# Performance work log

Measured on AMD Instinct MI355X. Metric: run time of the kernel, lower is better.

The kernel has to match this reference:

```python
import jax, jax.numpy as jnp
import numpy as np

SOS_TOKEN = 1


def gru_cell(x, h, Wih, Whh, bih, bhh):
    # torch.nn.GRU gate math; x:[B,H], h:[B,H]; Wih/Whh:[3H,H]
    gi = x @ Wih.T + bih
    gh = h @ Whh.T + bhh
    ir, iz, inn = jnp.split(gi, 3, axis=-1)
    hr, hz, hn = jnp.split(gh, 3, axis=-1)
    r = jax.nn.sigmoid(ir + hr)
    z = jax.nn.sigmoid(iz + hz)
    n = jnp.tanh(inn + r * hn)
    return (1.0 - z) * n + z * h


def setup_inputs() -> dict:
    key = jax.random.key(0)
    ks = jax.random.split(key, 20)
    B, S, T, V, H = 32, 512, 128, 32000, 512
    sc = 0.08
    p = lambda i, shape: (jax.random.normal(ks[i], shape, jnp.float32) * sc)
    return {
        "input_seq": jax.random.randint(ks[0], (B, S), 0, V),
        "target_seq": jax.random.randint(ks[1], (B, T), 0, V),
        "emb": p(2, (V, H)),
        "ef_Wih": p(3, (3 * H, H)), "ef_Whh": p(4, (3 * H, H)),
        "ef_bih": p(5, (3 * H,)), "ef_bhh": p(6, (3 * H,)),
        "eb_Wih": p(7, (3 * H, H)), "eb_Whh": p(8, (3 * H, H)),
        "eb_bih": p(9, (3 * H,)), "eb_bhh": p(10, (3 * H,)),
        "d_Wih": p(11, (3 * H, H)), "d_Whh": p(12, (3 * H, H)),
        "d_bih": p(13, (3 * H,)), "d_bhh": p(14, (3 * H,)),
        "att_W": p(15, (H, 2 * H)), "att_b": p(16, (H,)),
        "out_W": p(17, (V, H)), "out_b": p(18, (V,)),
    }


def reference(input_seq, target_seq, emb,
              ef_Wih, ef_Whh, ef_bih, ef_bhh,
              eb_Wih, eb_Whh, eb_bih, eb_bhh,
              d_Wih, d_Whh, d_bih, d_bhh,
              att_W, att_b, out_W, out_b):
    B, S = input_seq.shape
    T = target_seq.shape[1]
    H = emb.shape[1]
    dtype = emb.dtype

    # ---- encoder: bidirectional GRU over source ----
    xs = jnp.swapaxes(emb[input_seq], 0, 1)  # [S,B,H]
    h0 = jnp.zeros((B, H), dtype)

    def make_step(Wih, Whh, bih, bhh):
        def f(h, xt):
            hn = gru_cell(xt, h, Wih, Whh, bih, bhh)
            return hn, hn
        return f

    hf_last, out_f = jax.lax.scan(make_step(ef_Wih, ef_Whh, ef_bih, ef_bhh), h0, xs)
    hb_last, out_bwd = jax.lax.scan(make_step(eb_Wih, eb_Whh, eb_bih, eb_bhh), h0, xs[::-1])
    out_bwd = out_bwd[::-1]
    # encoder_output[:, :H] + encoder_output[:, H:]  == sum of directions
    enc_out = jnp.swapaxes(out_f + out_bwd, 0, 1)  # [B,S,H]
    # decoder_hidden = encoder_hidden[-1,0] + encoder_hidden[-1,1]
    h_dec0 = hf_last + hb_last  # [B,H]

    # ---- greedy decode for T steps with argmax feedback ----
    tgt = target_seq.T  # [T,B]
    tok0 = jnp.full((B,), SOS_TOKEN, target_seq.dtype)
    batch_idx = jnp.arange(B)

    def dec_step(carry, tgt_t):
        h, tok, loss = carry
        xt = emb[tok]                                   # [B,H]
        hn = gru_cell(xt, h, d_Wih, d_Whh, d_bih, d_bhh)
        scores = jnp.einsum('bh,bsh->bs', hn, enc_out)  # dot attention
        w = jax.nn.softmax(scores, axis=-1)
        ctx = jnp.einsum('bs,bsh->bh', w, enc_out)
        att_out = jnp.tanh(jnp.concatenate([ctx, hn], axis=-1) @ att_W.T + att_b)
        logits = att_out @ out_W.T + out_b              # [B,V]
        logp = jax.nn.log_softmax(logits, axis=-1)
        loss = loss - logp[batch_idx, tgt_t]            # -log softmax(output)[target]
        nxt = jnp.argmax(logits, axis=-1).astype(tok.dtype)
        return (hn, nxt, loss), None

    init = (h_dec0, tok0, jnp.zeros((B,), dtype))
    (_, _, loss), _ = jax.lax.scan(dec_step, init, tgt)
    # mean over examples of (per-example loss / decoding_cnt)
    return jnp.mean(loss / T)
```

## Files before the change

### kernel.cpp

```cpp
#include <hip/hip_runtime.h>
#include <math.h>

#define B 32
#define S 512
#define T 128
#define V 32000
#define H 512
#define NB 256
#define NTE 512
#define NTD 256
#define LCHUNK 250
#define LROWS 128

__device__ __forceinline__ float dot4(float acc, float4 a, float4 b){
    return fmaf(a.x,b.x, fmaf(a.y,b.y, fmaf(a.z,b.z, fmaf(a.w,b.w, acc))));
}
__device__ __forceinline__ float sigmoidf_(float x){ return 1.0f/(1.0f+expf(-x)); }

template<int GRPSZ>
__device__ __forceinline__ void gbar_arrive(unsigned* bb, unsigned grp, unsigned n){
    __syncthreads();
    if (threadIdx.x == 0){
        const unsigned r = __hip_atomic_fetch_add(bb + grp*32, 1u,
                              __ATOMIC_RELEASE, __HIP_MEMORY_SCOPE_AGENT);
        if (r == n*(unsigned)GRPSZ - 1u){
            const unsigned q = __hip_atomic_fetch_add(bb + 256, 1u,
                                  __ATOMIC_RELEASE, __HIP_MEMORY_SCOPE_AGENT);
            if (q == n*8u - 1u)
                __hip_atomic_store(bb + 288, n,
                                   __ATOMIC_RELEASE, __HIP_MEMORY_SCOPE_AGENT);
        }
    }
}
__device__ __forceinline__ void gbar_wait(unsigned* bb, unsigned n){
    if (threadIdx.x == 0){
        long guard = 0;
        while (__hip_atomic_load(bb + 288, __ATOMIC_RELAXED, __HIP_MEMORY_SCOPE_AGENT) < n){
            __builtin_amdgcn_s_sleep(2);
            if (++guard > 200000000L) break;
        }
        (void)__hip_atomic_load(bb + 288, __ATOMIC_ACQUIRE, __HIP_MEMORY_SCOPE_AGENT);
    }
    __syncthreads();
}

__global__ __launch_bounds__(NTE, 1) void enc_persistent(
    const int* __restrict__ input_seq, const float* __restrict__ emb,
    const float* __restrict__ fWih, const float* __restrict__ fWhh,
    const float* __restrict__ fbih, const float* __restrict__ fbhh,
    const float* __restrict__ bWih, const float* __restrict__ bWhh,
    const float* __restrict__ bbih, const float* __restrict__ bbhh,
    float* enc_out, float* out_b, unsigned* bars)
{
    __shared__ float wlds[24*512];
    __shared__ float shp[3*128*6];
    const int bk = blockIdx.x, tid = threadIdx.x;
    const int dir = bk & 1, jg = bk >> 1;
    const int b = tid & 31, jj = (tid>>5)&3, kh = tid>>7;
    const int j = jg*4 + jj;
    const unsigned grp = ((unsigned)jg) & 7u;

    const float *Wih = dir? bWih : fWih;
    const float *Whh = dir? bWhh : fWhh;
    const float *bih = dir? bbih : fbih;
    const float *bhh = dir? bbhh : fbhh;
    float* outp = dir? out_b : enc_out;
    unsigned* bar = bars + dir*1024;

    for (int r=0;r<24;r++){
        const int jr = jg*4 + (r/6);
        const int g  = r % 6;
        const float* src = (g<3) ? (Wih + ((size_t)g*H + jr)*H)
                                 : (Whh + ((size_t)(g-3)*H + jr)*H);
        for (int k=tid;k<H;k+=NTE) wlds[r*512+k] = src[k];
    }
    __syncthreads();

    const float4* wx0 = (const float4*)(wlds + (jj*6+0)*512 + kh*128);
    const float4* wx1 = (const float4*)(wlds + (jj*6+1)*512 + kh*128);
    const float4* wx2 = (const float4*)(wlds + (jj*6+2)*512 + kh*128);
    const float4* wh0 = (const float4*)(wlds + (jj*6+3)*512 + kh*128);
    const float4* wh1 = (const float4*)(wlds + (jj*6+4)*512 + kh*128);
    const float4* wh2 = (const float4*)(wlds + (jj*6+5)*512 + kh*128);
    const float bi_r = bih[j], bi_z = bih[H+j], bi_n = bih[2*H+j];
    const float bh_r = bhh[j], bh_z = bhh[H+j], bh_n = bhh[2*H+j];

    for (int t=0; t<S; t++){
        const int pos  = dir ? (S-1-t) : t;
        const int hpos = dir ? (S-t)   : (t-1);
        const int tokb = input_seq[b*S + pos];
        const float4* x4 = (const float4*)(emb + (size_t)tokb*H + kh*128);

        float ir=0.f, iz=0.f, in_=0.f;
        #pragma unroll 8
        for (int k=0;k<32;k++){
            const float4 xv = x4[k];
            ir  = dot4(ir , xv, wx0[k]);
            iz  = dot4(iz , xv, wx1[k]);
            in_ = dot4(in_, xv, wx2[k]);
        }

        if (t > 0) gbar_wait(bar, (unsigned)t);

        float hr=0.f, hz=0.f, hn=0.f;
        if (t > 0){
            const float4* h4 = (const float4*)(outp + ((size_t)b*S + hpos)*H + kh*128);
            #pragma unroll 8
            for (int k=0;k<32;k++){
                const float4 hv = h4[k];
                hr = dot4(hr, hv, wh0[k]);
                hz = dot4(hz, hv, wh1[k]);
                hn = dot4(hn, hv, wh2[k]);
            }
        }
        if (kh){
            float* p = shp + ((kh-1)*128 + jj*32 + b)*6;
            p[0]=ir; p[1]=iz; p[2]=in_; p[3]=hr; p[4]=hz; p[5]=hn;
        }
        __syncthreads();
        if (!kh){
            #pragma unroll
            for (int q=0;q<3;q++){
                const float* p = shp + (q*128 + jj*32 + b)*6;
                ir+=p[0]; iz+=p[1]; in_+=p[2]; hr+=p[3]; hz+=p[4]; hn+=p[5];
            }
            float hprev = (t>0) ? outp[((size_t)b*S + hpos)*H + j] : 0.0f;
            const float r = sigmoidf_(ir + bi_r + hr + bh_r);
            const float z = sigmoidf_(iz + bi_z + hz + bh_z);
            const float n = tanhf(in_ + bi_n + r*(hn + bh_n));
            outp[((size_t)b*S + pos)*H + j] = (1.0f - z)*n + z*hprev;
        }
        gbar_arrive<16>(bar, grp, (unsigned)(t+1));
    }
}

__global__ __launch_bounds__(NTD, 1) void dec_persistent(
    const int* __restrict__ target_seq, const float* __restrict__ emb,
    const float* __restrict__ dWih, const float* __restrict__ dWhh,
    const float* __restrict__ dbih, const float* __restrict__ dbhh,
    const float* __restrict__ attW, const float* __restrict__ attb,
    const float* __restrict__ outW, const float* __restrict__ outBias,
    float* enc_out, const float* out_b,
    float* hdec, float* scores, float* ctxb, float* att_out,
    float* pm, float* ps, int* pidx, float* lossb,
    float* out, unsigned* bar)
{
    __shared__ __align__(16) float smem[128*32*4];
    __shared__ float wg[12*512];
    __shared__ float wp[2*1024];
    __shared__ float red_m[4][32], red_s[4][32];
    __shared__ int   red_i[4][32];
    __shared__ int sh_tok[B];
    const int bk = blockIdx.x, tid = threadIdx.x;
    const unsigned grp = (unsigned)bk & 7u;
    unsigned bn = 1;
#define GSYNC() do { gbar_arrive<32>(bar, grp, bn); gbar_wait(bar, bn); ++bn; } while(0)

    for (int r=0;r<12;r++){
        const int jr = bk*2 + (r/6);
        const int g  = r % 6;
        const float* src = (g<3) ? (dWih + ((size_t)g*H + jr)*H)
                                 : (dWhh + ((size_t)(g-3)*H + jr)*H);
        for (int k=tid;k<H;k+=NTD) wg[r*512+k] = src[k];
    }
    for (int r=0;r<2;r++){
        const float* src = attW + (size_t)(bk*2+r)*(2*H);
        for (int k=tid;k<2*H;k+=NTD) wp[r*1024+k] = src[k];
    }

    {
        const int gid = bk*NTD + tid;
        if (gid < B*H){
            const int bb = gid >> 9, jq = gid & 511;
            hdec[gid] = enc_out[((size_t)bb*S + (S-1))*H + jq] + out_b[((size_t)bb*S)*H + jq];
        }
        if (bk==0 && tid<B) lossb[tid] = 0.0f;
    }
    GSYNC();

    {
        float4* e4 = (float4*)enc_out; const float4* o4 = (const float4*)out_b;
        for (size_t i = (size_t)bk*NTD + tid; i < (size_t)B*S*H/4; i += (size_t)NB*NTD){
            float4 x = e4[i]; const float4 y = o4[i];
            x.x+=y.x; x.y+=y.y; x.z+=y.z; x.w+=y.w; e4[i]=x;
        }
    }
    GSYNC();

    const int gb = tid & 31, gj = (tid>>5)&1, gkq = tid>>6;
    const int jrow = bk*2 + gj;
    const float4* gwir = (const float4*)(wg + (gj*6+0)*512 + gkq*128);
    const float4* gwiz = (const float4*)(wg + (gj*6+1)*512 + gkq*128);
    const float4* gwin = (const float4*)(wg + (gj*6+2)*512 + gkq*128);
    const float4* gwhr = (const float4*)(wg + (gj*6+3)*512 + gkq*128);
    const float4* gwhz = (const float4*)(wg + (gj*6+4)*512 + gkq*128);
    const float4* gwhn = (const float4*)(wg + (gj*6+5)*512 + gkq*128);
    const float gbi_r = dbih[jrow], gbi_z = dbih[H+jrow], gbi_n = dbih[2*H+jrow];
    const float gbh_r = dbhh[jrow], gbh_z = dbhh[H+jrow], gbh_n = dbhh[2*H+jrow];
    const float4* pw = (const float4*)(wp + gj*1024 + gkq*256);

    for (int t=0; t<T; t++){
        float* hin  = hdec + (size_t)(t&1)*B*H;
        float* hout = hdec + (size_t)((t+1)&1)*B*H;

        if (t == 0){
            if (tid < B) sh_tok[tid] = 1;
        } else {
            const int mb = tid>>3, p = tid&7;
            float bv = -INFINITY; int ai = 0x7FFFFFFF;
            for (int c=p; c<LCHUNK; c+=8){
                const float v = pm[mb*LCHUNK + c];
                if (v > bv){ bv = v; ai = pidx[mb*LCHUNK + c]; }
            }
            #pragma unroll
            for (int m=1; m<8; m<<=1){
                const float ov = __shfl_xor(bv, m); const int oi = __shfl_xor(ai, m);
                if (ov > bv || (ov == bv && oi < ai)){ bv = ov; ai = oi; }
            }
            if (p==0) sh_tok[mb] = ai;
            if (bk == 0){
                float mm = -INFINITY;
                for (int c=p; c<LCHUNK; c+=8) mm = fmaxf(mm, pm[mb*LCHUNK+c]);
                #pragma unroll
                for (int m=1;m<8;m<<=1) mm = fmaxf(mm, __shfl_xor(mm, m));
                float se = 0.0f;
                for (int c=p; c<LCHUNK; c+=8) se += ps[mb*LCHUNK+c]*expf(pm[mb*LCHUNK+c]-mm);
                #pragma unroll
                for (int m=1;m<8;m<<=1) se += __shfl_xor(se, m);
                const int tg = target_seq[mb*T + (t-1)];
                const float4* ar = (const float4*)(att_out + (size_t)mb*H) + p*16;
                const float4* wr = (const float4*)(outW + (size_t)tg*H) + p*16;
                float d = 0.0f;
                #pragma unroll
                for (int k=0;k<16;k++) d = dot4(d, ar[k], wr[k]);
                #pragma unroll
                for (int m=1;m<8;m<<=1) d += __shfl_xor(d, m);
                if (p==0) lossb[mb] += (mm + logf(se)) - (d + outBias[tg]);
            }
        }
        __syncthreads();
        {
            const int tokb = sh_tok[gb];
            const float4* x4 = (const float4*)(emb + (size_t)tokb*H + gkq*128);
            const float4* h4 = (const float4*)(hin + (size_t)gb*H + gkq*128);
            float ir=0.f, iz=0.f, in_=0.f, hr=0.f, hz=0.f, hn=0.f;
            #pragma unroll 4
            for (int k=0;k<32;k++){
                const float4 xv = x4[k], hv = h4[k];
                ir  = dot4(ir , xv, gwir[k]);
                iz  = dot4(iz , xv, gwiz[k]);
                in_ = dot4(in_, xv, gwin[k]);
                hr  = dot4(hr , hv, gwhr[k]);
                hz  = dot4(hz , hv, gwhz[k]);
                hn  = dot4(hn , hv, gwhn[k]);
            }
            if (gkq){
                float* pp = smem + ((gkq-1)*64 + gj*32 + gb)*6;
                pp[0]=ir; pp[1]=iz; pp[2]=in_; pp[3]=hr; pp[4]=hz; pp[5]=hn;
            }
            __syncthreads();
            if (!gkq){
                #pragma unroll
                for (int q=0;q<3;q++){
                    const float* pp = smem + (q*64 + gj*32 + gb)*6;
                    ir+=pp[0]; iz+=pp[1]; in_+=pp[2]; hr+=pp[3]; hz+=pp[4]; hn+=pp[5];
                }
                const float r = sigmoidf_(ir + gbi_r + hr + gbh_r);
                const float z = sigmoidf_(iz + gbi_z + hz + gbh_z);
                const float n = tanhf(in_ + gbi_n + r*(hn + gbh_n));
                const float hprev = hin[(size_t)gb*H + jrow];
                hout[(size_t)gb*H + jrow] = (1.0f - z)*n + z*hprev;
            }
        }
        GSYNC();

        {
            const int bS = bk & 31, sg = bk >> 5;
            const int sl = tid>>2, q = tid&3;
            const int s = sg*64 + sl;
            const float4* h4 = (const float4*)(hout + (size_t)bS*H + q*128);
            const float4* e4 = (const float4*)(enc_out + ((size_t)bS*S + s)*H + q*128);
            float a = 0.f;
            #pragma unroll 8
            for (int k=0;k<32;k++) a = dot4(a, h4[k], e4[k]);
            a += __shfl_xor(a, 1);
            a += __shfl_xor(a, 2);
            if (q == 0) scores[bS*S + s] = a;
        }
        GSYNC();

        {
            const int bC = bk & 31, cg = bk >> 5;
            float* sh_w = smem; float* red = smem + 512; float* part = smem + 768;
            const float s0 = scores[bC*S + tid], s1 = scores[bC*S + tid + 256];
            red[tid] = fmaxf(s0,s1); __syncthreads();
            for (int off=128; off>0; off>>=1){ if (tid<off) red[tid]=fmaxf(red[tid],red[tid+off]); __syncthreads(); }
            const float M = red[0]; __syncthreads();
            const float e0 = expf(s0-M), e1 = expf(s1-M);
            red[tid] = e0+e1; __syncthreads();
            for (int off=128; off>0; off>>=1){ if (tid<off) red[tid]+=red[tid+off]; __syncthreads(); }
            const float inv = 1.0f/red[0];
            __syncthreads();
            sh_w[tid] = e0*inv; sh_w[tid+256] = e1*inv;
            __syncthreads();
            const int col = cg*64 + (tid & 63);
            const int sg2 = tid >> 6;
            const float* Ec = enc_out + (size_t)bC*S*H + col;
            float acc = 0.f;
            #pragma unroll 8
            for (int s2=sg2; s2<S; s2+=4) acc = fmaf(sh_w[s2], Ec[(size_t)s2*H], acc);
            part[tid] = acc; __syncthreads();
            if (tid < 64) ctxb[bC*512 + col] = part[tid]+part[tid+64]+part[tid+128]+part[tid+192];
        }
        GSYNC();

        {
            const float* act = (gkq < 2) ? (ctxb + (size_t)gb*512 + gkq*256)
                                         : (hout + (size_t)gb*H + (gkq-2)*256);
            const float4* a4 = (const float4*)act;
            float acc = 0.f;
            #pragma unroll 8
            for (int k=0;k<64;k++) acc = dot4(acc, a4[k], pw[k]);
            if (gkq){
                smem[(gkq-1)*64 + gj*32 + gb] = acc;
            }
            __syncthreads();
            if (!gkq){
                acc += smem[0*64 + gj*32 + gb] + smem[1*64 + gj*32 + gb] + smem[2*64 + gj*32 + gb];
                att_out[(size_t)gb*H + jrow] = tanhf(acc + attb[jrow]);
            }
        }
        GSYNC();

        if (bk < LCHUNK){
            float4* sh4 = (float4*)smem;
            for (int idx = tid; idx < 32*128; idx += NTD){
                const int k4 = idx & 127, bb = idx >> 7;
                sh4[k4*32 + bb] = ((const float4*)att_out)[(size_t)bb*128 + k4];
            }
            __syncthreads();
            const int wid = tid >> 6, lane = tid & 63;
            const int rl = lane & 7, bl = lane >> 3;
            const int r0 = bk*LROWS + wid*32 + rl*4;
            const float4* w0 = (const float4*)(outW + (size_t)(r0+0)*H);
            const float4* w1 = (const float4*)(outW + (size_t)(r0+1)*H);
            const float4* w2 = (const float4*)(outW + (size_t)(r0+2)*H);
            const float4* w3 = (const float4*)(outW + (size_t)(r0+3)*H);
            float acc[4][4];
            #pragma unroll
            for (int i=0;i<4;i++){ acc[i][0]=0.f; acc[i][1]=0.f; acc[i][2]=0.f; acc[i][3]=0.f; }
            #pragma unroll 4
            for (int k=0;k<128;k++){
                const float4 a0 = sh4[k*32 + bl*4 + 0];
                const float4 a1 = sh4[k*32 + bl*4 + 1];
                const float4 a2 = sh4[k*32 + bl*4 + 2];
                const float4 a3 = sh4[k*32 + bl*4 + 3];
                {   const float4 wv = w0[k];
                    acc[0][0]=dot4(acc[0][0],wv,a0); acc[0][1]=dot4(acc[0][1],wv,a1);
                    acc[0][2]=dot4(acc[0][2],wv,a2); acc[0][3]=dot4(acc[0][3],wv,a3); }
                {   const float4 wv = w1[k];
                    acc[1][0]=dot4(acc[1][0],wv,a0); acc[1][1]=dot4(acc[1][1],wv,a1);
                    acc[1][2]=dot4(acc[1][2],wv,a2); acc[1][3]=dot4(acc[1][3],wv,a3); }
                {   const float4 wv = w2[k];
                    acc[2][0]=dot4(acc[2][0],wv,a0); acc[2][1]=dot4(acc[2][1],wv,a1);
                    acc[2][2]=dot4(acc[2][2],wv,a2); acc[2][3]=dot4(acc[2][3],wv,a3); }
                {   const float4 wv = w3[k];
                    acc[3][0]=dot4(acc[3][0],wv,a0); acc[3][1]=dot4(acc[3][1],wv,a1);
                    acc[3][2]=dot4(acc[3][2],wv,a2); acc[3][3]=dot4(acc[3][3],wv,a3); }
            }
            const float bs0 = outBias[r0], bs1 = outBias[r0+1], bs2 = outBias[r0+2], bs3 = outBias[r0+3];
            #pragma unroll
            for (int j=0;j<4;j++){
                const float l0 = acc[0][j]+bs0, l1 = acc[1][j]+bs1, l2 = acc[2][j]+bs2, l3 = acc[3][j]+bs3;
                float M = l0; int bi = r0;
                if (l1 > M){ M=l1; bi=r0+1; }
                if (l2 > M){ M=l2; bi=r0+2; }
                if (l3 > M){ M=l3; bi=r0+3; }
                float Ssum = expf(l0-M)+expf(l1-M)+expf(l2-M)+expf(l3-M);
                #pragma unroll
                for (int m=1;m<8;m<<=1){
                    const float oM = __shfl_xor(M, m);
                    const float oS = __shfl_xor(Ssum, m);
                    const int   oI = __shfl_xor(bi, m);
                    const float nM = fmaxf(M, oM);
                    const float nS = Ssum*expf(M-nM) + oS*expf(oM-nM);
                    if (oM > M || (oM == M && oI < bi)) bi = oI;
                    M = nM; Ssum = nS;
                }
                if (rl == 0){
                    red_m[wid][bl*4+j] = M;
                    red_s[wid][bl*4+j] = Ssum;
                    red_i[wid][bl*4+j] = bi;
                }
            }
            __syncthreads();
            if (tid < 32){
                float M = red_m[0][tid], Ssum = red_s[0][tid]; int bi = red_i[0][tid];
                #pragma unroll
                for (int w=1; w<4; w++){
                    const float oM = red_m[w][tid], oS = red_s[w][tid]; const int oI = red_i[w][tid];
                    const float nM = fmaxf(M, oM);
                    const float nS = Ssum*expf(M-nM) + oS*expf(oM-nM);
                    if (oM > M || (oM == M && oI < bi)) bi = oI;
                    M = nM; Ssum = nS;
                }
                pm[tid*LCHUNK + bk] = M;
                ps[tid*LCHUNK + bk] = Ssum;
                pidx[tid*LCHUNK + bk] = bi;
            }
        }
        GSYNC();
    }

    if (bk == 0){
        const int mb = tid>>3, p = tid&7;
        float mm = -INFINITY;
        for (int c=p; c<LCHUNK; c+=8) mm = fmaxf(mm, pm[mb*LCHUNK+c]);
        #pragma unroll
        for (int m=1;m<8;m<<=1) mm = fmaxf(mm, __shfl_xor(mm, m));
        float se = 0.0f;
        for (int c=p; c<LCHUNK; c+=8) se += ps[mb*LCHUNK+c]*expf(pm[mb*LCHUNK+c]-mm);
        #pragma unroll
        for (int m=1;m<8;m<<=1) se += __shfl_xor(se, m);
        const int tg = target_seq[mb*T + (T-1)];
        const float4* ar = (const float4*)(att_out + (size_t)mb*H) + p*16;
        const float4* wr = (const float4*)(outW + (size_t)tg*H) + p*16;
        float d = 0.0f;
        #pragma unroll
        for (int k=0;k<16;k++) d = dot4(d, ar[k], wr[k]);
        #pragma unroll
        for (int m=1;m<8;m<<=1) d += __shfl_xor(d, m);
        if (p==0) lossb[mb] += (mm + logf(se)) - (d + outBias[tg]);
        __syncthreads();
        if (tid < B){
            float v = lossb[tid];
            for (int off=16; off>0; off>>=1) v += __shfl_down(v, off);
            if (tid == 0) out[0] = v / (float)(B*T);
        }
    }
#undef GSYNC
}

extern "C" void kernel_launch(void* const* d_in, const int* in_sizes, int n_in,
                              void* d_out, int out_size, void* d_ws, size_t ws_size,
                              hipStream_t stream)
{
    const int*   input_seq  = (const int*)  d_in[0];
    const int*   target_seq = (const int*)  d_in[1];
    const float* emb    = (const float*)d_in[2];
    const float* efWih  = (const float*)d_in[3];
    const float* efWhh  = (const float*)d_in[4];
    const float* efbih  = (const float*)d_in[5];
    const float* efbhh  = (const float*)d_in[6];
    const float* ebWih  = (const float*)d_in[7];
    const float* ebWhh  = (const float*)d_in[8];
    const float* ebbih  = (const float*)d_in[9];
    const float* ebbhh  = (const float*)d_in[10];
    const float* dWih   = (const float*)d_in[11];
    const float* dWhh   = (const float*)d_in[12];
    const float* dbih   = (const float*)d_in[13];
    const float* dbhh   = (const float*)d_in[14];
    const float* attW   = (const float*)d_in[15];
    const float* attb   = (const float*)d_in[16];
    const float* outW   = (const float*)d_in[17];
    const float* outBias= (const float*)d_in[18];

    float* ws      = (float*)d_ws;
    unsigned* bars = (unsigned*)ws;
    float* enc_out = ws + 4096;
    float* outb    = enc_out + (size_t)B*S*H;
    float* scores  = outb    + (size_t)B*S*H;
    float* ctxb    = scores  + (size_t)B*S;
    float* attout  = ctxb    + (size_t)B*512;
    float* pm      = attout  + (size_t)B*H;
    float* ps      = pm      + (size_t)B*LCHUNK;
    int*   pidx    = (int*)(ps + (size_t)B*LCHUNK);
    float* hdec    = (float*)(pidx + (size_t)B*LCHUNK);
    float* lossb   = hdec    + (size_t)2*B*H;

    hipMemsetAsync(bars, 0, 16384, stream);

    enc_persistent<<<NB, NTE, 0, stream>>>(input_seq, emb,
        efWih, efWhh, efbih, efbhh, ebWih, ebWhh, ebbih, ebbhh,
        enc_out, outb, bars);

    dec_persistent<<<NB, NTD, 0, stream>>>(target_seq, emb,
        dWih, dWhh, dbih, dbhh, attW, attb, outW, outBias,
        enc_out, outb, hdec, scores, ctxb, attout,
        pm, ps, pidx, lossb, (float*)d_out, bars + 2048);
}
```

Measured before the change: 31.84 ms.

## Restructure decoder so one block per batch row does GRU, attention, projection locally

```diff
diff --git a/kernel.cpp b/kernel.cpp
--- a/kernel.cpp
+++ b/kernel.cpp
@@ -8,9 +8,10 @@
 #define H 512
 #define NB 256
 #define NTE 512
-#define NTD 256
+#define NTD 1024
 #define LCHUNK 250
 #define LROWS 128
+#define BPITCH 49
 
 __device__ __forceinline__ float dot4(float acc, float4 a, float4 b){
     return fmaf(a.x,b.x, fmaf(a.y,b.y, fmaf(a.z,b.z, fmaf(a.w,b.w, acc))));
@@ -141,40 +142,35 @@
     const float* __restrict__ attW, const float* __restrict__ attb,
     const float* __restrict__ outW, const float* __restrict__ outBias,
     float* enc_out, const float* out_b,
-    float* hdec, float* scores, float* ctxb, float* att_out,
-    float* pm, float* ps, int* pidx, float* lossb,
+    float* att_out, float* pm, float* ps, int* pidx, float* lossb,
     float* out, unsigned* bar)
 {
-    __shared__ __align__(16) float smem[128*32*4];
-    __shared__ float wg[12*512];
-    __shared__ float wp[2*1024];
-    __shared__ float red_m[4][32], red_s[4][32];
-    __shared__ int   red_i[4][32];
-    __shared__ int sh_tok[B];
+    __shared__ __align__(16) float smem[128*BPITCH*4];
+    __shared__ __align__(16) float P_H[2*512];
+    __shared__ __align__(16) float P_AO[512];
+    __shared__ float P_LOSS;
+    __shared__ int   P_TOK;
+    __shared__ float BR_M[8][32], BR_S[8][32];
+    __shared__ int   BR_I[8][32];
+
+    float* A_X   = smem;
+    float* A_P6  = smem + 512;
+    float* A_SC  = smem + 3584;
+    float* A_P1  = smem + 4096;
+    float* A_CTX = smem + 4608;
+    float* A_RED = smem + 5120;
+    int*   A_REDI= (int*)(smem + 5152);
+
     const int bk = blockIdx.x, tid = threadIdx.x;
     const unsigned grp = (unsigned)bk & 7u;
     unsigned bn = 1;
 #define GSYNC() do { gbar_arrive<32>(bar, grp, bn); gbar_wait(bar, bn); ++bn; } while(0)
 
-    for (int r=0;r<12;r++){
-        const int jr = bk*2 + (r/6);
-        const int g  = r % 6;
-        const float* src = (g<3) ? (dWih + ((size_t)g*H + jr)*H)
-                                 : (dWhh + ((size_t)(g-3)*H + jr)*H);
-        for (int k=tid;k<H;k+=NTD) wg[r*512+k] = src[k];
-    }
-    for (int r=0;r<2;r++){
-        const float* src = attW + (size_t)(bk*2+r)*(2*H);
-        for (int k=tid;k<2*H;k+=NTD) wp[r*1024+k] = src[k];
-    }
-
-    {
-        const int gid = bk*NTD + tid;
-        if (gid < B*H){
-            const int bb = gid >> 9, jq = gid & 511;
-            hdec[gid] = enc_out[((size_t)bb*S + (S-1))*H + jq] + out_b[((size_t)bb*S)*H + jq];
-        }
-        if (bk==0 && tid<B) lossb[tid] = 0.0f;
+    if (bk < B){
+        if (tid < 512)
+            P_H[tid] = enc_out[((size_t)bk*S + (S-1))*H + tid]
+                     + out_b [((size_t)bk*S + 0    )*H + tid];
+        if (tid == 0) P_LOSS = 0.0f;
     }
     GSYNC();
 
@@ -187,147 +183,180 @@
     }
     GSYNC();
 
-    const int gb = tid & 31, gj = (tid>>5)&1, gkq = tid>>6;
-    const int jrow = bk*2 + gj;
-    const float4* gwir = (const float4*)(wg + (gj*6+0)*512 + gkq*128);
-    const float4* gwiz = (const float4*)(wg + (gj*6+1)*512 + gkq*128);
-    const float4* gwin = (const float4*)(wg + (gj*6+2)*512 + gkq*128);
-    const float4* gwhr = (const float4*)(wg + (gj*6+3)*512 + gkq*128);
-    const float4* gwhz = (const float4*)(wg + (gj*6+4)*512 + gkq*128);
-    const float4* gwhn = (const float4*)(wg + (gj*6+5)*512 + gkq*128);
-    const float gbi_r = dbih[jrow], gbi_z = dbih[H+jrow], gbi_n = dbih[2*H+jrow];
-    const float gbh_r = dbhh[jrow], gbh_z = dbhh[H+jrow], gbh_n = dbhh[2*H+jrow];
-    const float4* pw = (const float4*)(wp + gj*1024 + gkq*256);
-
     for (int t=0; t<T; t++){
-        float* hin  = hdec + (size_t)(t&1)*B*H;
-        float* hout = hdec + (size_t)((t+1)&1)*B*H;
-
-        if (t == 0){
-            if (tid < B) sh_tok[tid] = 1;
-        } else {
-            const int mb = tid>>3, p = tid&7;
-            float bv = -INFINITY; int ai = 0x7FFFFFFF;
-            for (int c=p; c<LCHUNK; c+=8){
-                const float v = pm[mb*LCHUNK + c];
-                if (v > bv){ bv = v; ai = pidx[mb*LCHUNK + c]; }
-            }
-            #pragma unroll
-            for (int m=1; m<8; m<<=1){
-                const float ov = __shfl_xor(bv, m); const int oi = __shfl_xor(ai, m);
-                if (ov > bv || (ov == bv && oi < ai)){ bv = ov; ai = oi; }
-            }
-            if (p==0) sh_tok[mb] = ai;
-            if (bk == 0){
-                float mm = -INFINITY;
-                for (int c=p; c<LCHUNK; c+=8) mm = fmaxf(mm, pm[mb*LCHUNK+c]);
+        if (bk < B){
+            const int b = bk;
+            float* ph = P_H + (t&1)*512;
+            float* pn = P_H + ((t+1)&1)*512;
+
+            if (t > 0){
+                const int tg = target_seq[b*T + (t-1)];
+                if (tid < 128){
+                    const float4 av = ((const float4*)P_AO)[tid];
+                    const float4 wv = ((const float4*)(outW + (size_t)tg*H))[tid];
+                    float d = av.x*wv.x + av.y*wv.y + av.z*wv.z + av.w*wv.w;
+                    #pragma unroll
+                    for (int m=1;m<64;m<<=1) d += __shfl_xor(d, m);
+                    if ((tid&63)==0) A_RED[16 + (tid>>6)] = d;
+                }
+                float mm = -INFINITY, zz = 0.0f, bv = -INFINITY; int ai = 0x7FFFFFFF;
+                if (tid < 256){
+                    if (tid < LCHUNK){
+                        mm = pm[b*LCHUNK + tid]; zz = ps[b*LCHUNK + tid];
+                        bv = mm; ai = pidx[b*LCHUNK + tid];
+                    }
+                    #pragma unroll
+                    for (int m=1;m<64;m<<=1){
+                        const float omm = __shfl_xor(mm, m), ozz = __shfl_xor(zz, m);
+                        const float obv = __shfl_xor(bv, m); const int oai = __shfl_xor(ai, m);
+                        if (obv > bv || (obv == bv && oai < ai)){ bv = obv; ai = oai; }
+                        const float nm = fmaxf(mm, omm);
+                        const float w1 = (mm  > -INFINITY)? expf(mm -nm) : 0.0f;
+                        const float w2 = (omm > -INFINITY)? expf(omm-nm) : 0.0f;
+                        zz = zz*w1 + ozz*w2; mm = nm;
+                    }
+                    if ((tid&63)==0){
+                        const int w = tid>>6;
+                        A_RED[w] = mm; A_RED[4+w] = zz; A_RED[8+w] = bv; A_REDI[w] = ai;
+                    }
+                }
+                __syncthreads();
+                if (tid == 0){
+                    float M = A_RED[0], Z = A_RED[4], BV = A_RED[8]; int AI = A_REDI[0];
+                    #pragma unroll
+                    for (int w=1; w<4; w++){
+                        const float oM = A_RED[w], oZ = A_RED[4+w], oB = A_RED[8+w];
+                        const int oI = A_REDI[w];
+                        if (oB > BV || (oB == BV && oI < AI)){ BV = oB; AI = oI; }
+                        const float nm = fmaxf(M, oM);
+                        const float w1 = (M  > -INFINITY)? expf(M -nm) : 0.0f;
+                        const float w2 = (oM > -INFINITY)? expf(oM-nm) : 0.0f;
+                        Z = Z*w1 + oZ*w2; M = nm;
+                    }
+                    const float d = A_RED[16] + A_RED[17];
+                    P_LOSS += (M + logf(Z)) - (d + outBias[tg]);
+                    P_TOK = AI;
+                }
+            } else {
+                if (tid == 0) P_TOK = 1;
+            }
+            __syncthreads();
+
+            {
+                const int tok = P_TOK;
+                if (tid < 128)
+                    ((float4*)A_X)[tid] = ((const float4*)(emb + (size_t)tok*H))[tid];
+            }
+            __syncthreads();
+
+            {
+                const int j = tid & 511, hf = tid >> 9;
+                const float4* x4 = (const float4*)A_X + hf*64;
+                const float4* h4 = (const float4*)ph  + hf*64;
+                const float4* wi0 = (const float4*)(dWih + ((size_t)(0*H + j))*H) + hf*64;
+                const float4* wi1 = (const float4*)(dWih + ((size_t)(1*H + j))*H) + hf*64;
+                const float4* wi2 = (const float4*)(dWih + ((size_t)(2*H + j))*H) + hf*64;
+                const float4* wh0 = (const float4*)(dWhh + ((size_t)(0*H + j))*H) + hf*64;
+                const float4* wh1 = (const float4*)(dWhh + ((size_t)(1*H + j))*H) + hf*64;
+                const float4* wh2 = (const float4*)(dWhh + ((size_t)(2*H + j))*H) + hf*64;
+                float ir=0.f, iz=0.f, in_=0.f, hr=0.f, hz=0.f, hn=0.f;
+                #pragma unroll 4
+                for (int k=0;k<64;k++){
+                    const float4 xv = x4[k], hv = h4[k];
+                    ir  = dot4(ir , xv, wi0[k]);
+                    iz  = dot4(iz , xv, wi1[k]);
+                    in_ = dot4(in_, xv, wi2[k]);
+                    hr  = dot4(hr , hv, wh0[k]);
+                    hz  = dot4(hz , hv, wh1[k]);
+                    hn  = dot4(hn , hv, wh2[k]);
+                }
+                if (hf){
+                    float* pp = A_P6 + j*6;
+                    pp[0]=ir; pp[1]=iz; pp[2]=in_; pp[3]=hr; pp[4]=hz; pp[5]=hn;
+                }
+                __syncthreads();
+                if (!hf){
+                    const float* pp = A_P6 + j*6;
+                    ir+=pp[0]; iz+=pp[1]; in_+=pp[2]; hr+=pp[3]; hz+=pp[4]; hn+=pp[5];
+                    const float r = sigmoidf_(ir + dbih[j]     + hr + dbhh[j]);
+                    const float z = sigmoidf_(iz + dbih[H+j]   + hz + dbhh[H+j]);
+                    const float n = tanhf   (in_ + dbih[2*H+j] + r*(hn + dbhh[2*H+j]));
+                    pn[j] = (1.0f - z)*n + z*ph[j];
+                }
+                __syncthreads();
+            }
+
+            {
+                const int s = tid & 511, hf = tid >> 9;
+                const float4* e4 = (const float4*)(enc_out + ((size_t)b*S + s)*H) + hf*64;
+                const float4* h4 = (const float4*)pn + hf*64;
+                float a = 0.f;
+                #pragma unroll 8
+                for (int k=0;k<64;k++) a = dot4(a, h4[k], e4[k]);
+                if (hf) A_P1[s] = a;
+                __syncthreads();
+                if (!hf) A_SC[s] = a + A_P1[s];
+                __syncthreads();
+            }
+
+            {
+                float v = (tid < 512)? A_SC[tid] : -INFINITY;
+                float vm = v;
                 #pragma unroll
-                for (int m=1;m<8;m<<=1) mm = fmaxf(mm, __shfl_xor(mm, m));
-                float se = 0.0f;
-                for (int c=p; c<LCHUNK; c+=8) se += ps[mb*LCHUNK+c]*expf(pm[mb*LCHUNK+c]-mm);
+                for (int m=1;m<64;m<<=1) vm = fmaxf(vm, __shfl_xor(vm, m));
+                if (tid < 512 && (tid&63)==0) A_RED[tid>>6] = vm;
+                __syncthreads();
+                if (tid == 0){
+                    float M = A_RED[0];
+                    #pragma unroll
+                    for (int w=1;w<8;w++) M = fmaxf(M, A_RED[w]);
+                    A_RED[8] = M;
+                }
+                __syncthreads();
+                const float M = A_RED[8];
+                const float e = (tid < 512)? expf(v - M) : 0.0f;
+                float es = e;
                 #pragma unroll
-                for (int m=1;m<8;m<<=1) se += __shfl_xor(se, m);
-                const int tg = target_seq[mb*T + (t-1)];
-                const float4* ar = (const float4*)(att_out + (size_t)mb*H) + p*16;
-                const float4* wr = (const float4*)(outW + (size_t)tg*H) + p*16;
-                float d = 0.0f;
-                #pragma unroll
-                for (int k=0;k<16;k++) d = dot4(d, ar[k], wr[k]);
-                #pragma unroll
-                for (int m=1;m<8;m<<=1) d += __shfl_xor(d, m);
-                if (p==0) lossb[mb] += (mm + logf(se)) - (d + outBias[tg]);
-            }
-        }
-        __syncthreads();
-        {
-            const int tokb = sh_tok[gb];
-            const float4* x4 = (const float4*)(emb + (size_t)tokb*H + gkq*128);
-            const float4* h4 = (const float4*)(hin + (size_t)gb*H + gkq*128);
-            float ir=0.f, iz=0.f, in_=0.f, hr=0.f, hz=0.f, hn=0.f;
-            #pragma unroll 4
-            for (int k=0;k<32;k++){
-                const float4 xv = x4[k], hv = h4[k];
-                ir  = dot4(ir , xv, gwir[k]);
-                iz  = dot4(iz , xv, gwiz[k]);
-                in_ = dot4(in_, xv, gwin[k]);
-                hr  = dot4(hr , hv, gwhr[k]);
-                hz  = dot4(hz , hv, gwhz[k]);
-                hn  = dot4(hn , hv, gwhn[k]);
-            }
-            if (gkq){
-                float* pp = smem + ((gkq-1)*64 + gj*32 + gb)*6;
-                pp[0]=ir; pp[1]=iz; pp[2]=in_; pp[3]=hr; pp[4]=hz; pp[5]=hn;
-            }
-            __syncthreads();
-            if (!gkq){
-                #pragma unroll
-                for (int q=0;q<3;q++){
-                    const float* pp = smem + (q*64 + gj*32 + gb)*6;
-                    ir+=pp[0]; iz+=pp[1]; in_+=pp[2]; hr+=pp[3]; hz+=pp[4]; hn+=pp[5];
-                }
-                const float r = sigmoidf_(ir + gbi_r + hr + gbh_r);
-                const float z = sigmoidf_(iz + gbi_z + hz + gbh_z);
-                const float n = tanhf(in_ + gbi_n + r*(hn + gbh_n));
-                const float hprev = hin[(size_t)gb*H + jrow];
-                hout[(size_t)gb*H + jrow] = (1.0f - z)*n + z*hprev;
-            }
-        }
-        GSYNC();
-
-        {
-            const int bS = bk & 31, sg = bk >> 5;
-            const int sl = tid>>2, q = tid&3;
-            const int s = sg*64 + sl;
-            const float4* h4 = (const float4*)(hout + (size_t)bS*H + q*128);
-            const float4* e4 = (const float4*)(enc_out + ((size_t)bS*S + s)*H + q*128);
-            float a = 0.f;
-            #pragma unroll 8
-            for (int k=0;k<32;k++) a = dot4(a, h4[k], e4[k]);
-            a += __shfl_xor(a, 1);
-            a += __shfl_xor(a, 2);
-            if (q == 0) scores[bS*S + s] = a;
-        }
-        GSYNC();
-
-        {
-            const int bC = bk & 31, cg = bk >> 5;
-            float* sh_w = smem; float* red = smem + 512; float* part = smem + 768;
-            const float s0 = scores[bC*S + tid], s1 = scores[bC*S + tid + 256];
-            red[tid] = fmaxf(s0,s1); __syncthreads();
-            for (int off=128; off>0; off>>=1){ if (tid<off) red[tid]=fmaxf(red[tid],red[tid+off]); __syncthreads(); }
-            const float M = red[0]; __syncthreads();
-            const float e0 = expf(s0-M), e1 = expf(s1-M);
-            red[tid] = e0+e1; __syncthreads();
-            for (int off=128; off>0; off>>=1){ if (tid<off) red[tid]+=red[tid+off]; __syncthreads(); }
-            const float inv = 1.0f/red[0];
-            __syncthreads();
-            sh_w[tid] = e0*inv; sh_w[tid+256] = e1*inv;
-            __syncthreads();
-            const int col = cg*64 + (tid & 63);
-            const int sg2 = tid >> 6;
-            const float* Ec = enc_out + (size_t)bC*S*H + col;
-            float acc = 0.f;
-            #pragma unroll 8
-            for (int s2=sg2; s2<S; s2+=4) acc = fmaf(sh_w[s2], Ec[(size_t)s2*H], acc);
-            part[tid] = acc; __syncthreads();
-            if (tid < 64) ctxb[bC*512 + col] = part[tid]+part[tid+64]+part[tid+128]+part[tid+192];
-        }
-        GSYNC();
-
-        {
-            const float* act = (gkq < 2) ? (ctxb + (size_t)gb*512 + gkq*256)
-                                         : (hout + (size_t)gb*H + (gkq-2)*256);
-            const float4* a4 = (const float4*)act;
-            float acc = 0.f;
-            #pragma unroll 8
-            for (int k=0;k<64;k++) acc = dot4(acc, a4[k], pw[k]);
-            if (gkq){
-                smem[(gkq-1)*64 + gj*32 + gb] = acc;
-            }
-            __syncthreads();
-            if (!gkq){
-                acc += smem[0*64 + gj*32 + gb] + smem[1*64 + gj*32 + gb] + smem[2*64 + gj*32 + gb];
-                att_out[(size_t)gb*H + jrow] = tanhf(acc + attb[jrow]);
+                for (int m=1;m<64;m<<=1) es += __shfl_xor(es, m);
+                if (tid < 512 && (tid&63)==0) A_RED[16 + (tid>>6)] = es;
+                __syncthreads();
+                if (tid == 0){
+                    float Z = A_RED[16];
+                    #pragma unroll
+                    for (int w=1;w<8;w++) Z += A_RED[16+w];
+                    A_RED[9] = 1.0f/Z;
+                }
+                __syncthreads();
+                if (tid < 512) A_SC[tid] = e * A_RED[9];
+                __syncthreads();
+            }
+
+            {
+                const int c = tid & 511, hf = tid >> 9;
+                const float* Ec = enc_out + (size_t)b*S*H + c;
+                float acc = 0.f;
+                const int s0 = hf*256;
+                #pragma unroll 8
+                for (int s2=s0; s2<s0+256; ++s2) acc = fmaf(A_SC[s2], Ec[(size_t)s2*H], acc);
+                if (hf) A_P1[c] = acc;
+                __syncthreads();
+                if (!hf) A_CTX[c] = acc + A_P1[c];
+                __syncthreads();
+            }
+
+            {
+                const int r = tid & 511, hf = tid >> 9;
+                const float4* aw  = (const float4*)(attW + (size_t)r*(2*H) + hf*512);
+                const float4* cat = (const float4*)(hf ? pn : A_CTX);
+                float acc = 0.f;
+                #pragma unroll 8
+                for (int k=0;k<128;k++) acc = dot4(acc, cat[k], aw[k]);
+                if (hf) A_P1[r] = acc;
+                __syncthreads();
+                if (!hf) P_AO[r] = tanhf(acc + A_P1[r] + attb[r]);
+                __syncthreads();
+                if (tid < 128)
+                    ((float4*)att_out)[(size_t)b*128 + tid] = ((const float4*)P_AO)[tid];
             }
         }
         GSYNC();
@@ -336,107 +365,123 @@
             float4* sh4 = (float4*)smem;
             for (int idx = tid; idx < 32*128; idx += NTD){
                 const int k4 = idx & 127, bb = idx >> 7;
-                sh4[k4*32 + bb] = ((const float4*)att_out)[(size_t)bb*128 + k4];
+                sh4[k4*BPITCH + (bb>>1)*3 + (bb&1)] =
+                    ((const float4*)att_out)[(size_t)bb*128 + k4];
             }
             __syncthreads();
-            const int wid = tid >> 6, lane = tid & 63;
-            const int rl = lane & 7, bl = lane >> 3;
-            const int r0 = bk*LROWS + wid*32 + rl*4;
-            const float4* w0 = (const float4*)(outW + (size_t)(r0+0)*H);
-            const float4* w1 = (const float4*)(outW + (size_t)(r0+1)*H);
-            const float4* w2 = (const float4*)(outW + (size_t)(r0+2)*H);
-            const float4* w3 = (const float4*)(outW + (size_t)(r0+3)*H);
-            float acc[4][4];
-            #pragma unroll
-            for (int i=0;i<4;i++){ acc[i][0]=0.f; acc[i][1]=0.f; acc[i][2]=0.f; acc[i][3]=0.f; }
-            #pragma unroll 4
-            for (int k=0;k<128;k++){
-                const float4 a0 = sh4[k*32 + bl*4 + 0];
-                const float4 a1 = sh4[k*32 + bl*4 + 1];
-                const float4 a2 = sh4[k*32 + bl*4 + 2];
-                const float4 a3 = sh4[k*32 + bl*4 + 3];
-                {   const float4 wv = w0[k];
-                    acc[0][0]=dot4(acc[0][0],wv,a0); acc[0][1]=dot4(acc[0][1],wv,a1);
-                    acc[0][2]=dot4(acc[0][2],wv,a2); acc[0][3]=dot4(acc[0][3],wv,a3); }
-                {   const float4 wv = w1[k];
-                    acc[1][0]=dot4(acc[1][0],wv,a0); acc[1][1]=dot4(acc[1][1],wv,a1);
-                    acc[1][2]=dot4(acc[1][2],wv,a2); acc[1][3]=dot4(acc[1][3],wv,a3); }
-                {   const float4 wv = w2[k];
-                    acc[2][0]=dot4(acc[2][0],wv,a0); acc[2][1]=dot4(acc[2][1],wv,a1);
-                    acc[2][2]=dot4(acc[2][2],wv,a2); acc[2][3]=dot4(acc[2][3],wv,a3); }
-                {   const float4 wv = w3[k];
-                    acc[3][0]=dot4(acc[3][0],wv,a0); acc[3][1]=dot4(acc[3][1],wv,a1);
-                    acc[3][2]=dot4(acc[3][2],wv,a2); acc[3][3]=dot4(acc[3][3],wv,a3); }
-            }
-            const float bs0 = outBias[r0], bs1 = outBias[r0+1], bs2 = outBias[r0+2], bs3 = outBias[r0+3];
-            #pragma unroll
-            for (int j=0;j<4;j++){
-                const float l0 = acc[0][j]+bs0, l1 = acc[1][j]+bs1, l2 = acc[2][j]+bs2, l3 = acc[3][j]+bs3;
-                float M = l0; int bi = r0;
-                if (l1 > M){ M=l1; bi=r0+1; }
-                if (l2 > M){ M=l2; bi=r0+2; }
-                if (l3 > M){ M=l3; bi=r0+3; }
-                float Ssum = expf(l0-M)+expf(l1-M)+expf(l2-M)+expf(l3-M);
+            if (tid < 512){
+                const int w = tid >> 6, lane = tid & 63;
+                const int rq = lane & 3, bg = lane >> 2;
+                const int r0 = bk*LROWS + w*16 + rq*4;
+                const float4* w0 = (const float4*)(outW + (size_t)(r0+0)*H);
+                const float4* w1 = (const float4*)(outW + (size_t)(r0+1)*H);
+                const float4* w2 = (const float4*)(outW + (size_t)(r0+2)*H);
+                const float4* w3 = (const float4*)(outW + (size_t)(r0+3)*H);
+                float acc[4][2];
                 #pragma unroll
-                for (int m=1;m<8;m<<=1){
-                    const float oM = __shfl_xor(M, m);
-                    const float oS = __shfl_xor(Ssum, m);
-                    const int   oI = __shfl_xor(bi, m);
-                    const float nM = fmaxf(M, oM);
-                    const float nS = Ssum*expf(M-nM) + oS*expf(oM-nM);
-                    if (oM > M || (oM == M && oI < bi)) bi = oI;
-                    M = nM; Ssum = nS;
-                }
-                if (rl == 0){
-                    red_m[wid][bl*4+j] = M;
-                    red_s[wid][bl*4+j] = Ssum;
-                    red_i[wid][bl*4+j] = bi;
+                for (int i=0;i<4;i++){ acc[i][0]=0.f; acc[i][1]=0.f; }
+                #pragma unroll 4
+                for (int k=0;k<128;k++){
+                    const float4 a0 = sh4[k*BPITCH + bg*3 + 0];
+                    const float4 a1 = sh4[k*BPITCH + bg*3 + 1];
+                    const float4 v0 = w0[k], v1 = w1[k], v2 = w2[k], v3 = w3[k];
+                    acc[0][0]=dot4(acc[0][0],v0,a0); acc[0][1]=dot4(acc[0][1],v0,a1);
+                    acc[1][0]=dot4(acc[1][0],v1,a0); acc[1][1]=dot4(acc[1][1],v1,a1);
+                    acc[2][0]=dot4(acc[2][0],v2,a0); acc[2][1]=dot4(acc[2][1],v2,a1);
+                    acc[3][0]=dot4(acc[3][0],v3,a0); acc[3][1]=dot4(acc[3][1],v3,a1);
+                }
+                const float bs0 = outBias[r0], bs1 = outBias[r0+1],
+                            bs2 = outBias[r0+2], bs3 = outBias[r0+3];
+                #pragma unroll
+                for (int j=0;j<2;j++){
+                    const float l0 = acc[0][j]+bs0, l1 = acc[1][j]+bs1,
+                                l2 = acc[2][j]+bs2, l3 = acc[3][j]+bs3;
+                    float M = l0; int bi = r0;
+                    if (l1 > M){ M=l1; bi=r0+1; }
+                    if (l2 > M){ M=l2; bi=r0+2; }
+                    if (l3 > M){ M=l3; bi=r0+3; }
+                    float Z = expf(l0-M)+expf(l1-M)+expf(l2-M)+expf(l3-M);
+                    #pragma unroll
+                    for (int m=1;m<4;m<<=1){
+                        const float oM = __shfl_xor(M, m);
+                        const float oZ = __shfl_xor(Z, m);
+                        const int   oI = __shfl_xor(bi, m);
+                        const float nm = fmaxf(M, oM);
+                        const float q1 = expf(M-nm), q2 = expf(oM-nm);
+                        if (oM > M || (oM == M && oI < bi)) bi = oI;
+                        Z = Z*q1 + oZ*q2; M = nm;
+                    }
+                    if (rq == 0){
+                        const int bb = bg*2 + j;
+                        BR_M[w][bb] = M; BR_S[w][bb] = Z; BR_I[w][bb] = bi;
+                    }
                 }
             }
             __syncthreads();
             if (tid < 32){
-                float M = red_m[0][tid], Ssum = red_s[0][tid]; int bi = red_i[0][tid];
+                float M = BR_M[0][tid], Z = BR_S[0][tid]; int bi = BR_I[0][tid];
                 #pragma unroll
-                for (int w=1; w<4; w++){
-                    const float oM = red_m[w][tid], oS = red_s[w][tid]; const int oI = red_i[w][tid];
-                    const float nM = fmaxf(M, oM);
-                    const float nS = Ssum*expf(M-nM) + oS*expf(oM-nM);
+                for (int w=1; w<8; w++){
+                    const float oM = BR_M[w][tid], oZ = BR_S[w][tid];
+                    const int oI = BR_I[w][tid];
+                    const float nm = fmaxf(M, oM);
+                    const float q1 = expf(M-nm), q2 = expf(oM-nm);
                     if (oM > M || (oM == M && oI < bi)) bi = oI;
-                    M = nM; Ssum = nS;
+                    Z = Z*q1 + oZ*q2; M = nm;
                 }
                 pm[tid*LCHUNK + bk] = M;
-                ps[tid*LCHUNK + bk] = Ssum;
+                ps[tid*LCHUNK + bk] = Z;
                 pidx[tid*LCHUNK + bk] = bi;
             }
         }
         GSYNC();
     }
 
-    if (bk == 0){
-        const int mb = tid>>3, p = tid&7;
-        float mm = -INFINITY;
-        for (int c=p; c<LCHUNK; c+=8) mm = fmaxf(mm, pm[mb*LCHUNK+c]);
-        #pragma unroll
-        for (int m=1;m<8;m<<=1) mm = fmaxf(mm, __shfl_xor(mm, m));
-        float se = 0.0f;
-        for (int c=p; c<LCHUNK; c+=8) se += ps[mb*LCHUNK+c]*expf(pm[mb*LCHUNK+c]-mm);
-        #pragma unroll
-        for (int m=1;m<8;m<<=1) se += __shfl_xor(se, m);
-        const int tg = target_seq[mb*T + (T-1)];
-        const float4* ar = (const float4*)(att_out + (size_t)mb*H) + p*16;
-        const float4* wr = (const float4*)(outW + (size_t)tg*H) + p*16;
-        float d = 0.0f;
-        #pragma unroll
-        for (int k=0;k<16;k++) d = dot4(d, ar[k], wr[k]);
-        #pragma unroll
-        for (int m=1;m<8;m<<=1) d += __shfl_xor(d, m);
-        if (p==0) lossb[mb] += (mm + logf(se)) - (d + outBias[tg]);
+    if (bk < B){
+        const int b = bk;
+        const int tg = target_seq[b*T + (T-1)];
+        if (tid < 128){
+            const float4 av = ((const float4*)P_AO)[tid];
+            const float4 wv = ((const float4*)(outW + (size_t)tg*H))[tid];
+            float d = av.x*wv.x + av.y*wv.y + av.z*wv.z + av.w*wv.w;
+            #pragma unroll
+            for (int m=1;m<64;m<<=1) d += __shfl_xor(d, m);
+            if ((tid&63)==0) A_RED[16 + (tid>>6)] = d;
+        }
+        float mm = -INFINITY, zz = 0.0f;
+        if (tid < 256){
+            if (tid < LCHUNK){ mm = pm[b*LCHUNK + tid]; zz = ps[b*LCHUNK + tid]; }
+            #pragma unroll
+            for (int m=1;m<64;m<<=1){
+                const float omm = __shfl_xor(mm, m), ozz = __shfl_xor(zz, m);
+                const float nm = fmaxf(mm, omm);
+                const float w1 = (mm  > -INFINITY)? expf(mm -nm) : 0.0f;
+                const float w2 = (omm > -INFINITY)? expf(omm-nm) : 0.0f;
+                zz = zz*w1 + ozz*w2; mm = nm;
+            }
+            if ((tid&63)==0){ const int w = tid>>6; A_RED[w] = mm; A_RED[4+w] = zz; }
+        }
         __syncthreads();
-        if (tid < B){
-            float v = lossb[tid];
-            for (int off=16; off>0; off>>=1) v += __shfl_down(v, off);
-            if (tid == 0) out[0] = v / (float)(B*T);
-        }
+        if (tid == 0){
+            float M = A_RED[0], Z = A_RED[4];
+            #pragma unroll
+            for (int w=1; w<4; w++){
+                const float oM = A_RED[w], oZ = A_RED[4+w];
+                const float nm = fmaxf(M, oM);
+                const float w1 = (M  > -INFINITY)? expf(M -nm) : 0.0f;
+                const float w2 = (oM > -INFINITY)? expf(oM-nm) : 0.0f;
+                Z = Z*w1 + oZ*w2; M = nm;
+            }
+            const float d = A_RED[16] + A_RED[17];
+            lossb[b] = P_LOSS + (M + logf(Z)) - (d + outBias[tg]);
+        }
+    }
+    GSYNC();
+
+    if (bk == 0 && tid < B){
+        float v = lossb[tid];
+        for (int off=16; off>0; off>>=1) v += __shfl_down(v, off);
+        if (tid == 0) out[0] = v / (float)(B*T);
     }
 #undef GSYNC
 }
@@ -469,14 +514,11 @@
     unsigned* bars = (unsigned*)ws;
     float* enc_out = ws + 4096;
     float* outb    = enc_out + (size_t)B*S*H;
-    float* scores  = outb    + (size_t)B*S*H;
-    float* ctxb    = scores  + (size_t)B*S;
-    float* attout  = ctxb    + (size_t)B*512;
+    float* attout  = outb    + (size_t)B*S*H;
     float* pm      = attout  + (size_t)B*H;
     float* ps      = pm      + (size_t)B*LCHUNK;
     int*   pidx    = (int*)(ps + (size_t)B*LCHUNK);
-    float* hdec    = (float*)(pidx + (size_t)B*LCHUNK);
-    float* lossb   = hdec    + (size_t)2*B*H;
+    float* lossb   = (float*)(pidx + (size_t)B*LCHUNK);
 
     hipMemsetAsync(bars, 0, 16384, stream);
 
@@ -486,6 +528,6 @@
 
     dec_persistent<<<NB, NTD, 0, stream>>>(target_seq, emb,
         dWih, dWhh, dbih, dbhh, attW, attb, outW, outBias,
-        enc_out, outb, hdec, scores, ctxb, attout,
-        pm, ps, pidx, lossb, (float*)d_out, bars + 2048);
+        enc_out, outb, attout, pm, ps, pidx, lossb,
+        (float*)d_out, bars + 2048);
 }
```

Result: slower. 68.58 ms (+115.4%).

## Stage encoder inputs/hidden in LDS, coalesce attention scores, pad logits LDS tile

Applied to the files above, without the earlier changes.

```diff
diff --git a/kernel.cpp b/kernel.cpp
--- a/kernel.cpp
+++ b/kernel.cpp
@@ -11,6 +11,7 @@
 #define NTD 256
 #define LCHUNK 250
 #define LROWS 128
+#define XPITCH 520
 
 __device__ __forceinline__ float dot4(float acc, float4 a, float4 b){
     return fmaf(a.x,b.x, fmaf(a.y,b.y, fmaf(a.z,b.z, fmaf(a.w,b.w, acc))));
@@ -54,6 +55,7 @@
 {
     __shared__ float wlds[24*512];
     __shared__ float shp[3*128*6];
+    __shared__ float xh[32*XPITCH];
     const int bk = blockIdx.x, tid = threadIdx.x;
     const int dir = bk & 1, jg = bk >> 1;
     const int b = tid & 31, jj = (tid>>5)&3, kh = tid>>7;
@@ -88,23 +90,42 @@
     for (int t=0; t<S; t++){
         const int pos  = dir ? (S-1-t) : t;
         const int hpos = dir ? (S-t)   : (t-1);
-        const int tokb = input_seq[b*S + pos];
-        const float4* x4 = (const float4*)(emb + (size_t)tokb*H + kh*128);
+
+        #pragma unroll
+        for (int it=0; it<8; ++it){
+            const int idx = it*NTE + tid;
+            const int bb = idx >> 7, c = idx & 127;
+            const int tok = input_seq[bb*S + pos];
+            ((float4*)(xh + bb*XPITCH))[c] =
+                ((const float4*)(emb + (size_t)tok*H))[c];
+        }
+        __syncthreads();
 
         float ir=0.f, iz=0.f, in_=0.f;
-        #pragma unroll 8
-        for (int k=0;k<32;k++){
-            const float4 xv = x4[k];
-            ir  = dot4(ir , xv, wx0[k]);
-            iz  = dot4(iz , xv, wx1[k]);
-            in_ = dot4(in_, xv, wx2[k]);
+        {
+            const float4* x4 = (const float4*)(xh + b*XPITCH + kh*128);
+            #pragma unroll 8
+            for (int k=0;k<32;k++){
+                const float4 xv = x4[k];
+                ir  = dot4(ir , xv, wx0[k]);
+                iz  = dot4(iz , xv, wx1[k]);
+                in_ = dot4(in_, xv, wx2[k]);
+            }
         }
 
         if (t > 0) gbar_wait(bar, (unsigned)t);
 
-        float hr=0.f, hz=0.f, hn=0.f;
+        float hr=0.f, hz=0.f, hn=0.f, hprev = 0.f;
         if (t > 0){
-            const float4* h4 = (const float4*)(outp + ((size_t)b*S + hpos)*H + kh*128);
+            #pragma unroll
+            for (int it=0; it<8; ++it){
+                const int idx = it*NTE + tid;
+                const int bb = idx >> 7, c = idx & 127;
+                ((float4*)(xh + bb*XPITCH))[c] =
+                    ((const float4*)(outp + ((size_t)bb*S + hpos)*H))[c];
+            }
+            __syncthreads();
+            const float4* h4 = (const float4*)(xh + b*XPITCH + kh*128);
             #pragma unroll 8
             for (int k=0;k<32;k++){
                 const float4 hv = h4[k];
@@ -112,6 +133,7 @@
                 hz = dot4(hz, hv, wh1[k]);
                 hn = dot4(hn, hv, wh2[k]);
             }
+            hprev = xh[b*XPITCH + j];
         }
         if (kh){
             float* p = shp + ((kh-1)*128 + jj*32 + b)*6;
@@ -124,7 +146,6 @@
                 const float* p = shp + (q*128 + jj*32 + b)*6;
                 ir+=p[0]; iz+=p[1]; in_+=p[2]; hr+=p[3]; hz+=p[4]; hn+=p[5];
             }
-            float hprev = (t>0) ? outp[((size_t)b*S + hpos)*H + j] : 0.0f;
             const float r = sigmoidf_(ir + bi_r + hr + bh_r);
             const float z = sigmoidf_(iz + bi_z + hz + bh_z);
             const float n = tanhf(in_ + bi_n + r*(hn + bh_n));
@@ -145,7 +166,7 @@
     float* pm, float* ps, int* pidx, float* lossb,
     float* out, unsigned* bar)
 {
-    __shared__ __align__(16) float smem[128*32*4];
+    __shared__ __align__(16) float smem[128*33*4];
     __shared__ float wg[12*512];
     __shared__ float wp[2*1024];
     __shared__ float red_m[4][32], red_s[4][32];
@@ -276,16 +297,25 @@
 
         {
             const int bS = bk & 31, sg = bk >> 5;
-            const int sl = tid>>2, q = tid&3;
-            const int s = sg*64 + sl;
-            const float4* h4 = (const float4*)(hout + (size_t)bS*H + q*128);
-            const float4* e4 = (const float4*)(enc_out + ((size_t)bS*S + s)*H + q*128);
-            float a = 0.f;
-            #pragma unroll 8
-            for (int k=0;k<32;k++) a = dot4(a, h4[k], e4[k]);
-            a += __shfl_xor(a, 1);
-            a += __shfl_xor(a, 2);
-            if (q == 0) scores[bS*S + s] = a;
+            if (tid < 128)
+                ((float4*)smem)[tid] = ((const float4*)(hout + (size_t)bS*H))[tid];
+            __syncthreads();
+            const int w = tid >> 6, lane = tid & 63;
+            const float4 h0 = ((const float4*)smem)[lane];
+            const float4 h1 = ((const float4*)smem)[64 + lane];
+            const int sbase = sg*64 + w*16;
+            #pragma unroll 4
+            for (int i=0;i<16;i++){
+                const int s = sbase + i;
+                const float4* e4 = (const float4*)(enc_out + ((size_t)bS*S + s)*H);
+                const float4 e0 = e4[lane], e1 = e4[64+lane];
+                float a = 0.f;
+                a = dot4(a, e0, h0);
+                a = dot4(a, e1, h1);
+                #pragma unroll
+                for (int m=1;m<64;m<<=1) a += __shfl_xor(a, m);
+                if (lane == 0) scores[bS*S + s] = a;
+            }
         }
         GSYNC();
 
@@ -336,7 +366,7 @@
             float4* sh4 = (float4*)smem;
             for (int idx = tid; idx < 32*128; idx += NTD){
                 const int k4 = idx & 127, bb = idx >> 7;
-                sh4[k4*32 + bb] = ((const float4*)att_out)[(size_t)bb*128 + k4];
+                sh4[k4*33 + bb] = ((const float4*)att_out)[(size_t)bb*128 + k4];
             }
             __syncthreads();
             const int wid = tid >> 6, lane = tid & 63;
@@ -351,10 +381,10 @@
             for (int i=0;i<4;i++){ acc[i][0]=0.f; acc[i][1]=0.f; acc[i][2]=0.f; acc[i][3]=0.f; }
             #pragma unroll 4
             for (int k=0;k<128;k++){
-                const float4 a0 = sh4[k*32 + bl*4 + 0];
-                const float4 a1 = sh4[k*32 + bl*4 + 1];
-                const float4 a2 = sh4[k*32 + bl*4 + 2];
-                const float4 a3 = sh4[k*32 + bl*4 + 3];
+                const float4 a0 = sh4[k*33 + bl*4 + 0];
+                const float4 a1 = sh4[k*33 + bl*4 + 1];
+                const float4 a2 = sh4[k*33 + bl*4 + 2];
+                const float4 a3 = sh4[k*33 + bl*4 + 3];
                 {   const float4 wv = w0[k];
                     acc[0][0]=dot4(acc[0][0],wv,a0); acc[0][1]=dot4(acc[0][1],wv,a1);
                     acc[0][2]=dot4(acc[0][2],wv,a2); acc[0][3]=dot4(acc[0][3],wv,a3); }
```

New measurement: 30.10 ms. 1.06x faster.
